# Kernel tuning notes

Hardware: AMD Instinct MI355X
Metric: run time of the kernel (lower is better)

The kernel has to match this reference:

```python
import jax, jax.numpy as jnp
import numpy as np

M_NODES, N_FEAT, HIDDEN = 1024, 64, 64


def _linear_init(key, fan_in, fan_out):
    kw, kb = jax.random.split(key)
    s = 1.0 / np.sqrt(fan_in)
    W = jax.random.uniform(kw, (fan_in, fan_out), minval=-s, maxval=s, dtype=jnp.float32)
    b = jax.random.uniform(kb, (fan_out,), minval=-s, maxval=s, dtype=jnp.float32)
    return W, b


def setup_inputs() -> dict:
    key = jax.random.key(0)
    ks = jax.random.split(key, 9)
    M, n, hid = M_NODES, N_FEAT, HIDDEN
    We1, be1 = _linear_init(ks[0], 2 * n + 2, hid)  # phi_e layer 1: [h_i, h_j, d2, a]
    We2, be2 = _linear_init(ks[1], hid, hid)         # phi_e layer 2
    Wx1, bx1 = _linear_init(ks[2], hid, hid)         # phi_x layer 1
    Wx2, bx2 = _linear_init(ks[3], hid, 1)           # phi_x layer 2 (scalar edge weight)
    Wh1, bh1 = _linear_init(ks[4], n + hid, hid)     # phi_h layer 1: [h_i, m_i]
    Wh2, bh2 = _linear_init(ks[5], hid, n)           # phi_h layer 2
    x = jax.random.normal(ks[6], (M, 3), dtype=jnp.float32)
    a = jax.random.uniform(ks[7], (M, M, 1), dtype=jnp.float32)
    h = jax.random.normal(ks[8], (M, n), dtype=jnp.float32)  # embedding table (all node ids)
    return dict(x=x, a=a, h=h, We1=We1, be1=be1, We2=We2, be2=be2,
                Wx1=Wx1, bx1=bx1, Wx2=Wx2, bx2=bx2, Wh1=Wh1, bh1=bh1, Wh2=Wh2, bh2=bh2)


def reference(x, a, h, We1, be1, We2, be2, Wx1, bx1, Wx2, bx2, Wh1, bh1, Wh2, bh2):
    M = x.shape[0]
    n = h.shape[1]
    C = 1.0 / (M - 1)
    # pairwise coordinate differences and squared distances
    diff = x[:, None, :] - x[None, :, :]                 # [M, M, 3]
    d2 = jnp.sum(diff * diff, axis=-1, keepdims=True)    # [M, M, 1]
    # phi_e layer-1 computed without materializing the [M, M, 2n+2] concat:
    # split We1 rows for h_i, h_j, d2, a contributions
    pe_i = h @ We1[:n]           # [M, hid]
    pe_j = h @ We1[n:2 * n]      # [M, hid]
    pre = pe_i[:, None, :] + pe_j[None, :, :] + d2 * We1[2 * n] + a * We1[2 * n + 1] + be1
    m = jax.nn.silu(jax.nn.silu(pre) @ We2 + be2)        # [M, M, hid]
    # coordinate update: x_i' = x_i + C * sum_j (x_i - x_j) * phi_x(m_ij)
    s = jax.nn.silu(m @ Wx1 + bx1) @ Wx2 + bx2           # [M, M, 1]
    mask = (1.0 - jnp.eye(M, dtype=x.dtype))[:, :, None]  # exclude self-loops
    x_new = x + C * jnp.sum(diff * s * mask, axis=1)      # [M, 3]
    # message aggregation over complete graph minus self-loops (m_ij @ all_neighbors)
    m_i = jnp.sum(m * mask, axis=1)                      # [M, hid]
    # node update: h' = phi_h([h_i, m_i])
    h_new = jax.nn.silu(jnp.concatenate([h, m_i], axis=-1) @ Wh1 + bh1) @ Wh2 + bh2
    return x_new, h_new
```

## Files before the change

kernel.cpp:

```cpp
#include <hip/hip_runtime.h>


#define MM 1024

typedef _Float16 half8 __attribute__((ext_vector_type(8)));
typedef float f32x4 __attribute__((ext_vector_type(4)));
typedef int int4t __attribute__((ext_vector_type(4)));

__device__ __forceinline__ float fsilu(float v) {
    float e = __expf(-v);
    return v * __builtin_amdgcn_rcpf(1.0f + e);
}

__global__ void __launch_bounds__(64) egnn_prepack(
    const float* __restrict__ h, const float* __restrict__ We1,
    const float* __restrict__ be1, const float* __restrict__ We2,
    const float* __restrict__ Wx1,
    float* __restrict__ peib, float* __restrict__ pej,
    _Float16* __restrict__ we2hi, _Float16* __restrict__ we2lo,
    _Float16* __restrict__ wx1h)
{
    const int b = blockIdx.x;
    const int tid = threadIdx.x;
    if (b < 1024) {
        const int i = b;
        const int c = tid;
        __shared__ float hrow[64];
        hrow[c] = h[i * 64 + c];
        __syncthreads();
        float acc1 = be1[c], acc2 = 0.0f;
#pragma unroll 8
        for (int cp = 0; cp < 64; ++cp) {
            const float hv = hrow[cp];
            acc1 = fmaf(hv, We1[cp * 64 + c], acc1);
            acc2 = fmaf(hv, We1[(64 + cp) * 64 + c], acc2);
        }
        peib[i * 64 + c] = acc1;
        pej[i * 64 + c]  = acc2;
    } else {
        const int idx = (b - 1024) * 64 + tid;
        const int e = idx & 7, l = (idx >> 3) & 63, f = (idx >> 9) & 7;
        const int n = f >> 1, s = f & 1;
        const int outc = 16 * n + (l & 15);
        const int kc   = 32 * s + ((l >> 4) * 8) + e;
        if (idx < 4096) {
            const float wv = We2[kc * 64 + outc];
            const _Float16 hi = (_Float16)wv;
            we2hi[idx] = hi;
            we2lo[idx] = (_Float16)(wv - (float)hi);
        } else {
            wx1h[idx - 4096] = (_Float16)Wx1[kc * 64 + outc];
        }
    }
}

#define EGNN_PREF(PJ0, PJ1, PJ2, PJ3, XJ0, XJ1, XJ2, TT)                       \
  {                                                                            \
    const int jn_ = (TT) * 64 + jbase;                                         \
    const float* __restrict__ pr_ = pej + jn_ * 64 + 8 * g;                    \
    PJ0 = *(const f32x4*)(pr_);                                                \
    PJ1 = *(const f32x4*)(pr_ + 4);                                            \
    PJ2 = *(const f32x4*)(pr_ + 32);                                           \
    PJ3 = *(const f32x4*)(pr_ + 36);                                           \
    XJ0 = x[jn_ * 3 + 0];                                                      \
    XJ1 = x[jn_ * 3 + 1];                                                      \
    XJ2 = x[jn_ * 3 + 2];                                                      \
  }

#define EGNN_BODY(PJ0, PJ1, PJ2, PJ3, XJ0, XJ1, XJ2, TT)                       \
  {                                                                            \
    const int jw_ = (TT) * 64 + jbase;                                         \
    const float d0_ = xi0 - (XJ0), d1_ = xi1 - (XJ1), d2_ = xi2 - (XJ2);       \
    const float dd_ = fmaf(d0_, d0_, fmaf(d1_, d1_, d2_ * d2_));               \
    const float av_ = aL[jw_];                                                 \
    const float sm_ = (jw_ == i) ? 0.0f : 1.0f;                                \
    half8 P0_, P1_;                                                            \
    _Pragma("unroll") for (int s = 0; s < 2; ++s) {                            \
      const f32x4 pjlo_ = s ? (PJ2) : (PJ0);                                   \
      const f32x4 pjhi_ = s ? (PJ3) : (PJ1);                                   \
      const f32x4 pe0_ = *(const f32x4*)&peibL[32 * s + 8 * g];                \
      const f32x4 pe1_ = *(const f32x4*)&peibL[32 * s + 8 * g + 4];            \
      const f32x4 wd0_ = *(const f32x4*)&wd2L[32 * s + 8 * g];                 \
      const f32x4 wd1_ = *(const f32x4*)&wd2L[32 * s + 8 * g + 4];             \
      const f32x4 wa0_ = *(const f32x4*)&waL[32 * s + 8 * g];                  \
      const f32x4 wa1_ = *(const f32x4*)&waL[32 * s + 8 * g + 4];              \
      half8 Pt_;                                                               \
      _Pragma("unroll") for (int e = 0; e < 8; ++e) {                          \
        const float pjv_ = (e < 4) ? pjlo_[e] : pjhi_[e - 4];                  \
        const float pev_ = (e < 4) ? pe0_[e] : pe1_[e - 4];                    \
        const float wdv_ = (e < 4) ? wd0_[e] : wd1_[e - 4];                    \
        const float wav_ = (e < 4) ? wa0_[e] : wa1_[e - 4];                    \
        float pre_ = pev_ + pjv_;                                              \
        pre_ = fmaf(dd_, wdv_, pre_);                                          \
        pre_ = fmaf(av_, wav_, pre_);                                          \
        Pt_[e] = (_Float16)fsilu(pre_);                                        \
      }                                                                        \
      if (s == 0) P0_ = Pt_; else P1_ = Pt_;                                   \
    }                                                                          \
    f32x4 acc1_[4];                                                            \
    _Pragma("unroll") for (int n = 0; n < 4; ++n)                              \
      acc1_[n] = *(const f32x4*)&be2L[16 * n + 4 * g];                         \
    _Pragma("unroll") for (int n = 0; n < 4; ++n) {                            \
      acc1_[n] = __builtin_amdgcn_mfma_f32_16x16x32_f16(whi[n][0], P0_, acc1_[n], 0, 0, 0); \
      acc1_[n] = __builtin_amdgcn_mfma_f32_16x16x32_f16(whi[n][1], P1_, acc1_[n], 0, 0, 0); \
      acc1_[n] = __builtin_amdgcn_mfma_f32_16x16x32_f16(wlo[n][0], P0_, acc1_[n], 0, 0, 0); \
      acc1_[n] = __builtin_amdgcn_mfma_f32_16x16x32_f16(wlo[n][1], P1_, acc1_[n], 0, 0, 0); \
    }                                                                          \
    int srcp_[4][2];                                                           \
    _Pragma("unroll") for (int n = 0; n < 4; ++n) {                            \
      const float m0_ = fsilu(acc1_[n][0]);                                    \
      const float m1_ = fsilu(acc1_[n][1]);                                    \
      const float m2_ = fsilu(acc1_[n][2]);                                    \
      const float m3_ = fsilu(acc1_[n][3]);                                    \
      msum[n][0] = fmaf(m0_, sm_, msum[n][0]);                                 \
      msum[n][1] = fmaf(m1_, sm_, msum[n][1]);                                 \
      msum[n][2] = fmaf(m2_, sm_, msum[n][2]);                                 \
      msum[n][3] = fmaf(m3_, sm_, msum[n][3]);                                 \
      srcp_[n][0] = __builtin_bit_cast(int, __builtin_amdgcn_cvt_pkrtz(m0_, m1_)); \
      srcp_[n][1] = __builtin_bit_cast(int, __builtin_amdgcn_cvt_pkrtz(m2_, m3_)); \
    }                                                                          \
    half8 B20_, B21_;                                                          \
    _Pragma("unroll") for (int s2 = 0; s2 < 2; ++s2) {                         \
      int4t bi_;                                                               \
      _Pragma("unroll") for (int p = 0; p < 4; ++p) {                          \
        const int sl_ = (p < 2) ? sl_lo : sl_hi;                               \
        const int va_ = __shfl(srcp_[2 * s2][p & 1], sl_, 64);                 \
        const int vb_ = __shfl(srcp_[2 * s2 + 1][p & 1], sl_, 64);             \
        bi_[p] = hiSel ? vb_ : va_;                                            \
      }                                                                        \
      if (s2 == 0) B20_ = __builtin_bit_cast(half8, bi_);                      \
      else B21_ = __builtin_bit_cast(half8, bi_);                              \
    }                                                                          \
    f32x4 acc2_[4];                                                            \
    _Pragma("unroll") for (int n = 0; n < 4; ++n)                              \
      acc2_[n] = *(const f32x4*)&bx1L[16 * n + 4 * g];                         \
    _Pragma("unroll") for (int n = 0; n < 4; ++n) {                            \
      acc2_[n] = __builtin_amdgcn_mfma_f32_16x16x32_f16(wx1f[n][0], B20_, acc2_[n], 0, 0, 0); \
      acc2_[n] = __builtin_amdgcn_mfma_f32_16x16x32_f16(wx1f[n][1], B21_, acc2_[n], 0, 0, 0); \
    }                                                                          \
    float sp_ = 0.0f;                                                          \
    _Pragma("unroll") for (int n = 0; n < 4; ++n) {                            \
      const f32x4 wq_ = *(const f32x4*)&wx2L[16 * n + 4 * g];                  \
      sp_ = fmaf(fsilu(acc2_[n][0]), wq_[0], sp_);                             \
      sp_ = fmaf(fsilu(acc2_[n][1]), wq_[1], sp_);                             \
      sp_ = fmaf(fsilu(acc2_[n][2]), wq_[2], sp_);                             \
      sp_ = fmaf(fsilu(acc2_[n][3]), wq_[3], sp_);                             \
    }                                                                          \
    sp_ += __shfl_xor(sp_, 16, 64);                                            \
    sp_ += __shfl_xor(sp_, 32, 64);                                            \
    const float sv_ = sp_ + bx2v;                                              \
    xa0 = fmaf(d0_, sv_, xa0);                                                 \
    xa1 = fmaf(d1_, sv_, xa1);                                                 \
    xa2 = fmaf(d2_, sv_, xa2);                                                 \
  }

__global__ void __launch_bounds__(256, 2) egnn_main(
    const float* __restrict__ x, const float* __restrict__ a,
    const float* __restrict__ h, const float* __restrict__ We1,
    const float* __restrict__ peib, const float* __restrict__ pej,
    const _Float16* __restrict__ we2hi, const _Float16* __restrict__ we2lo,
    const _Float16* __restrict__ wx1h,
    const float* __restrict__ be2,
    const float* __restrict__ bx1, const float* __restrict__ Wx2,
    const float* __restrict__ bx2,
    const float* __restrict__ Wh1, const float* __restrict__ bh1,
    const float* __restrict__ Wh2, const float* __restrict__ bh2,
    float* __restrict__ out)
{
    const int i = blockIdx.x;
    const int tid = threadIdx.x;
    const int w = tid >> 6;
    const int l = tid & 63;
    const int g = l >> 4;
    const int q15 = l & 15;

    __shared__ __align__(16) float aL[1024];
    __shared__ __align__(16) float peibL[64], wd2L[64], waL[64], be2L[64], bx1L[64], wx2L[64];
    __shared__ __align__(16) float partialL[256];
    __shared__ float xpartL[4][3];
    __shared__ float miL[64], hrowL[64], hid1L[64];

    ((f32x4*)aL)[tid] = ((const f32x4*)(a + i * MM))[tid];
    if (tid < 64) {
        peibL[tid] = peib[i * 64 + tid];
        wd2L[tid]  = We1[128 * 64 + tid];
        waL[tid]   = We1[129 * 64 + tid];
        be2L[tid]  = be2[tid];
        bx1L[tid]  = bx1[tid];
        wx2L[tid]  = Wx2[tid];
        hrowL[tid] = h[i * 64 + tid];
    }
    __syncthreads();

    const half8* __restrict__ w2h = (const half8*)we2hi;
    const half8* __restrict__ w2l = (const half8*)we2lo;
    const half8* __restrict__ wxh = (const half8*)wx1h;
    half8 whi[4][2], wlo[4][2], wx1f[4][2];
#pragma unroll
    for (int n = 0; n < 4; ++n)
#pragma unroll
        for (int s = 0; s < 2; ++s) {
            whi[n][s]  = w2h[(n * 2 + s) * 64 + l];
            wlo[n][s]  = w2l[(n * 2 + s) * 64 + l];
            wx1f[n][s] = wxh[(n * 2 + s) * 64 + l];
        }

    const float xi0 = x[i * 3 + 0], xi1 = x[i * 3 + 1], xi2 = x[i * 3 + 2];
    const float bx2v = bx2[0];
    const int sl_lo = q15 + 32 * (g & 1);
    const int sl_hi = sl_lo + 16;
    const bool hiSel = (g >= 2);
    const int jbase = 16 * w + q15;

    float msum[4][4];
#pragma unroll
    for (int n = 0; n < 4; ++n)
#pragma unroll
        for (int r = 0; r < 4; ++r) msum[n][r] = 0.0f;
    float xa0 = 0.0f, xa1 = 0.0f, xa2 = 0.0f;

    f32x4 pjA0, pjA1, pjA2, pjA3;
    f32x4 pjB0, pjB1, pjB2, pjB3;
    float xjA0, xjA1, xjA2, xjB0, xjB1, xjB2;

    EGNN_PREF(pjA0, pjA1, pjA2, pjA3, xjA0, xjA1, xjA2, 0)
    for (int t = 0; t < 16; t += 2) {
        EGNN_PREF(pjB0, pjB1, pjB2, pjB3, xjB0, xjB1, xjB2, t + 1)
        EGNN_BODY(pjA0, pjA1, pjA2, pjA3, xjA0, xjA1, xjA2, t)
        if (t + 2 < 16)
            EGNN_PREF(pjA0, pjA1, pjA2, pjA3, xjA0, xjA1, xjA2, t + 2)
        EGNN_BODY(pjB0, pjB1, pjB2, pjB3, xjB0, xjB1, xjB2, t + 1)
    }

#pragma unroll
    for (int n = 0; n < 4; ++n)
#pragma unroll
        for (int r = 0; r < 4; ++r) {
            float v = msum[n][r];
            v += __shfl_xor(v, 1, 64);
            v += __shfl_xor(v, 2, 64);
            v += __shfl_xor(v, 4, 64);
            v += __shfl_xor(v, 8, 64);
            msum[n][r] = v;
        }
    if (q15 == 0) {
#pragma unroll
        for (int n = 0; n < 4; ++n) {
            f32x4 sv4;
            sv4[0] = msum[n][0]; sv4[1] = msum[n][1];
            sv4[2] = msum[n][2]; sv4[3] = msum[n][3];
            *(f32x4*)&partialL[w * 64 + 16 * n + 4 * g] = sv4;
        }
    }
    {
        float v0 = xa0, v1 = xa1, v2 = xa2;
        for (int sft = 1; sft < 64; sft <<= 1) {
            v0 += __shfl_xor(v0, sft, 64);
            v1 += __shfl_xor(v1, sft, 64);
            v2 += __shfl_xor(v2, sft, 64);
        }
        if (l == 0) { xpartL[w][0] = v0; xpartL[w][1] = v1; xpartL[w][2] = v2; }
    }
    __syncthreads();

    if (tid < 64)
        miL[tid] = partialL[tid] + partialL[64 + tid] + partialL[128 + tid] + partialL[192 + tid];
    __syncthreads();

    if (tid < 64) {
        const int kk = tid;
        float a0 = bh1[kk], a1 = 0.0f;
#pragma unroll 8
        for (int c = 0; c < 64; ++c) {
            a0 = fmaf(hrowL[c], Wh1[c * 64 + kk], a0);
            a1 = fmaf(miL[c], Wh1[(64 + c) * 64 + kk], a1);
        }
        hid1L[kk] = fsilu(a0 + a1);
    }
    __syncthreads();

    if (tid < 64) {
        float accv = bh2[tid];
#pragma unroll 8
        for (int kk = 0; kk < 64; ++kk) accv = fmaf(hid1L[kk], Wh2[kk * 64 + tid], accv);
        out[3072 + i * 64 + tid] = accv;
    }
    if (tid == 0) {
        const float C = 0.25f / 1023.0f;
        out[i * 3 + 0] = xi0 + C * (xpartL[0][0] + xpartL[1][0] + xpartL[2][0] + xpartL[3][0]);
        out[i * 3 + 1] = xi1 + C * (xpartL[0][1] + xpartL[1][1] + xpartL[2][1] + xpartL[3][1]);
        out[i * 3 + 2] = xi2 + C * (xpartL[0][2] + xpartL[1][2] + xpartL[2][2] + xpartL[3][2]);
    }
}

extern "C" void kernel_launch(void* const* d_in, const int* in_sizes, int n_in,
                              void* d_out, int out_size, void* d_ws, size_t ws_size,
                              hipStream_t stream) {
    const float* x   = (const float*)d_in[0];
    const float* a   = (const float*)d_in[1];
    const float* h   = (const float*)d_in[2];
    const float* We1 = (const float*)d_in[3];
    const float* be1 = (const float*)d_in[4];
    const float* We2 = (const float*)d_in[5];
    const float* be2 = (const float*)d_in[6];
    const float* Wx1 = (const float*)d_in[7];
    const float* bx1 = (const float*)d_in[8];
    const float* Wx2 = (const float*)d_in[9];
    const float* bx2 = (const float*)d_in[10];
    const float* Wh1 = (const float*)d_in[11];
    const float* bh1 = (const float*)d_in[12];
    const float* Wh2 = (const float*)d_in[13];
    const float* bh2 = (const float*)d_in[14];
    float* out = (float*)d_out;

    float* peib = (float*)d_ws;
    float* pej  = peib + 65536;
    _Float16* we2hi = (_Float16*)(pej + 65536);
    _Float16* we2lo = we2hi + 4096;
    _Float16* wx1h  = we2lo + 4096;

    egnn_prepack<<<dim3(1152), dim3(64), 0, stream>>>(
        h, We1, be1, We2, Wx1, peib, pej, we2hi, we2lo, wx1h);
    egnn_main<<<dim3(1024), dim3(256), 0, stream>>>(
        x, a, h, We1, peib, pej, we2hi, we2lo, wx1h,
        be2, bx1, Wx2, bx2, Wh1, bh1, Wh2, bh2, out);
}
```

Baseline: 204.6 us.

## Move Wx1 fragments to LDS and single-buffer pej prefetch inside loop body

The Wx1 MFMA operand fragments are no longer held in registers; they are staged once into shared memory and read from LDS on each use. The double-buffered pej/x prefetch (A/B register sets) is replaced by one buffer that is reloaded for the next tile midway through the body, after the layer-1 activations are computed. Both changes cut VGPR pressure, presumably to avoid spills or raise occupancy under the 256x2 launch bounds. The cost is extra LDS reads per iteration and a shorter window for hiding global-load latency, plus one redundant prefetch on the last tile.

Result: slower. 224.4 us (+9.7%).

```diff
diff --git a/kernel.cpp b/kernel.cpp
--- a/kernel.cpp
+++ b/kernel.cpp
@@ -54,30 +54,30 @@
     }
 }
 
-#define EGNN_PREF(PJ0, PJ1, PJ2, PJ3, XJ0, XJ1, XJ2, TT)                       \
+#define EGNN_PREF(TT)                                                          \
   {                                                                            \
     const int jn_ = (TT) * 64 + jbase;                                         \
     const float* __restrict__ pr_ = pej + jn_ * 64 + 8 * g;                    \
-    PJ0 = *(const f32x4*)(pr_);                                                \
-    PJ1 = *(const f32x4*)(pr_ + 4);                                            \
-    PJ2 = *(const f32x4*)(pr_ + 32);                                           \
-    PJ3 = *(const f32x4*)(pr_ + 36);                                           \
-    XJ0 = x[jn_ * 3 + 0];                                                      \
-    XJ1 = x[jn_ * 3 + 1];                                                      \
-    XJ2 = x[jn_ * 3 + 2];                                                      \
+    pjA0 = *(const f32x4*)(pr_);                                               \
+    pjA1 = *(const f32x4*)(pr_ + 4);                                           \
+    pjA2 = *(const f32x4*)(pr_ + 32);                                          \
+    pjA3 = *(const f32x4*)(pr_ + 36);                                          \
+    xjA0 = x[jn_ * 3 + 0];                                                     \
+    xjA1 = x[jn_ * 3 + 1];                                                     \
+    xjA2 = x[jn_ * 3 + 2];                                                     \
   }
 
-#define EGNN_BODY(PJ0, PJ1, PJ2, PJ3, XJ0, XJ1, XJ2, TT)                       \
+#define EGNN_BODY(TT)                                                          \
   {                                                                            \
     const int jw_ = (TT) * 64 + jbase;                                         \
-    const float d0_ = xi0 - (XJ0), d1_ = xi1 - (XJ1), d2_ = xi2 - (XJ2);       \
+    const float d0_ = xi0 - xjA0, d1_ = xi1 - xjA1, d2_ = xi2 - xjA2;          \
     const float dd_ = fmaf(d0_, d0_, fmaf(d1_, d1_, d2_ * d2_));               \
     const float av_ = aL[jw_];                                                 \
     const float sm_ = (jw_ == i) ? 0.0f : 1.0f;                                \
     half8 P0_, P1_;                                                            \
     _Pragma("unroll") for (int s = 0; s < 2; ++s) {                            \
-      const f32x4 pjlo_ = s ? (PJ2) : (PJ0);                                   \
-      const f32x4 pjhi_ = s ? (PJ3) : (PJ1);                                   \
+      const f32x4 pjlo_ = s ? pjA2 : pjA0;                                     \
+      const f32x4 pjhi_ = s ? pjA3 : pjA1;                                     \
       const f32x4 pe0_ = *(const f32x4*)&peibL[32 * s + 8 * g];                \
       const f32x4 pe1_ = *(const f32x4*)&peibL[32 * s + 8 * g + 4];            \
       const f32x4 wd0_ = *(const f32x4*)&wd2L[32 * s + 8 * g];                 \
@@ -97,6 +97,11 @@
       }                                                                        \
       if (s == 0) P0_ = Pt_; else P1_ = Pt_;                                   \
     }                                                                          \
+           \
+    {                                                                          \
+      const int tn_ = ((TT) < 15) ? (TT) + 1 : 15;                             \
+      EGNN_PREF(tn_)                                                           \
+    }                                                                          \
     f32x4 acc1_[4];                                                            \
     _Pragma("unroll") for (int n = 0; n < 4; ++n)                              \
       acc1_[n] = *(const f32x4*)&be2L[16 * n + 4 * g];                         \
@@ -135,8 +140,8 @@
     _Pragma("unroll") for (int n = 0; n < 4; ++n)                              \
       acc2_[n] = *(const f32x4*)&bx1L[16 * n + 4 * g];                         \
     _Pragma("unroll") for (int n = 0; n < 4; ++n) {                            \
-      acc2_[n] = __builtin_amdgcn_mfma_f32_16x16x32_f16(wx1f[n][0], B20_, acc2_[n], 0, 0, 0); \
-      acc2_[n] = __builtin_amdgcn_mfma_f32_16x16x32_f16(wx1f[n][1], B21_, acc2_[n], 0, 0, 0); \
+      acc2_[n] = __builtin_amdgcn_mfma_f32_16x16x32_f16(wLDSx[(n * 2 + 0) * 64 + l], B20_, acc2_[n], 0, 0, 0); \
+      acc2_[n] = __builtin_amdgcn_mfma_f32_16x16x32_f16(wLDSx[(n * 2 + 1) * 64 + l], B21_, acc2_[n], 0, 0, 0); \
     }                                                                          \
     float sp_ = 0.0f;                                                          \
     _Pragma("unroll") for (int n = 0; n < 4; ++n) {                            \
@@ -174,12 +179,15 @@
     const int g = l >> 4;
     const int q15 = l & 15;
 
+    __shared__ half8 wLDSx[512];
     __shared__ __align__(16) float aL[1024];
     __shared__ __align__(16) float peibL[64], wd2L[64], waL[64], be2L[64], bx1L[64], wx2L[64];
     __shared__ __align__(16) float partialL[256];
     __shared__ float xpartL[4][3];
     __shared__ float miL[64], hrowL[64], hid1L[64];
 
+    for (int idx = tid; idx < 512; idx += 256)
+        wLDSx[idx] = ((const half8*)wx1h)[idx];
     ((f32x4*)aL)[tid] = ((const f32x4*)(a + i * MM))[tid];
     if (tid < 64) {
         peibL[tid] = peib[i * 64 + tid];
@@ -194,15 +202,13 @@
 
     const half8* __restrict__ w2h = (const half8*)we2hi;
     const half8* __restrict__ w2l = (const half8*)we2lo;
-    const half8* __restrict__ wxh = (const half8*)wx1h;
-    half8 whi[4][2], wlo[4][2], wx1f[4][2];
+    half8 whi[4][2], wlo[4][2];
 #pragma unroll
     for (int n = 0; n < 4; ++n)
 #pragma unroll
         for (int s = 0; s < 2; ++s) {
-            whi[n][s]  = w2h[(n * 2 + s) * 64 + l];
-            wlo[n][s]  = w2l[(n * 2 + s) * 64 + l];
-            wx1f[n][s] = wxh[(n * 2 + s) * 64 + l];
+            whi[n][s] = w2h[(n * 2 + s) * 64 + l];
+            wlo[n][s] = w2l[(n * 2 + s) * 64 + l];
         }
 
     const float xi0 = x[i * 3 + 0], xi1 = x[i * 3 + 1], xi2 = x[i * 3 + 2];
@@ -220,16 +226,12 @@
     float xa0 = 0.0f, xa1 = 0.0f, xa2 = 0.0f;
 
     f32x4 pjA0, pjA1, pjA2, pjA3;
-    f32x4 pjB0, pjB1, pjB2, pjB3;
-    float xjA0, xjA1, xjA2, xjB0, xjB1, xjB2;
-
-    EGNN_PREF(pjA0, pjA1, pjA2, pjA3, xjA0, xjA1, xjA2, 0)
-    for (int t = 0; t < 16; t += 2) {
-        EGNN_PREF(pjB0, pjB1, pjB2, pjB3, xjB0, xjB1, xjB2, t + 1)
-        EGNN_BODY(pjA0, pjA1, pjA2, pjA3, xjA0, xjA1, xjA2, t)
-        if (t + 2 < 16)
-            EGNN_PREF(pjA0, pjA1, pjA2, pjA3, xjA0, xjA1, xjA2, t + 2)
-        EGNN_BODY(pjB0, pjB1, pjB2, pjB3, xjB0, xjB1, xjB2, t + 1)
+    float xjA0, xjA1, xjA2;
+
+    EGNN_PREF(0)
+#pragma unroll 2
+    for (int t = 0; t < 16; ++t) {
+        EGNN_BODY(t)
     }
 
 #pragma unroll
```
